# Performance work log

Hardware: AMD Instinct MI355X
Metric: run time of the kernel (lower is better)

Reference implementation:

```python
import jax, jax.numpy as jnp
import numpy as np

B, S, E, H = 32, 4096, 256, 8
P, M = 256, 16  # positions per batch row, tokens per position (pileup depth)


def setup_inputs() -> dict:
    key = jax.random.key(0)
    k1, k2, k3, k4, k5, k6 = jax.random.split(key, 6)
    embeddings = jax.random.normal(k1, (B, S, E), jnp.float32)
    # each position 0..P-1 appears exactly M times per batch row, shuffled
    base = jnp.repeat(jnp.arange(P, dtype=jnp.int32), M)  # (S,)
    positions = jax.vmap(lambda k: jax.random.permutation(k, base))(jax.random.split(k2, B))
    scale = 1.0 / np.sqrt(E)
    Wq = jax.random.normal(k3, (E, E), jnp.float32) * scale
    Wk = jax.random.normal(k4, (E, E), jnp.float32) * scale
    Wv = jax.random.normal(k5, (E, E), jnp.float32) * scale
    W0 = jax.random.normal(k6, (E, E), jnp.float32) * scale
    return {"embeddings": embeddings, "Wq": Wq, "Wk": Wk, "Wv": Wv, "W0": W0,
            "positions": positions, "num_positions": P, "group_size": M, "num_heads": H}


def _intra_group_rank(positions):
    # rank[b,i] = number of earlier tokens j<i in row b with the same position
    Bb, Ss = positions.shape
    idx = jnp.arange(Ss)
    order = jnp.argsort(positions, axis=1)  # stable sort preserves original order within a group
    sp = jnp.take_along_axis(positions, order, axis=1)
    new_group = jnp.concatenate([jnp.ones((Bb, 1), bool), sp[:, 1:] != sp[:, :-1]], axis=1)
    group_start = jax.lax.cummax(jnp.where(new_group, idx[None, :], 0), axis=1)
    rank_sorted = idx[None, :] - group_start
    rank = jnp.zeros_like(positions).at[jnp.arange(Bb)[:, None], order].set(rank_sorted.astype(positions.dtype))
    return rank


def reference(embeddings, Wq, Wk, Wv, W0, positions, num_positions, group_size, num_heads):
    Bb, Ss, Ee = embeddings.shape
    Pp, Mm, Hh = num_positions, group_size, num_heads
    dh = Ee // Hh
    G = Bb * Pp

    valid = positions >= 0
    rank = _intra_group_rank(positions)                       # (B,S) slot within group
    gid = jnp.arange(Bb, dtype=positions.dtype)[:, None] * Pp + jnp.clip(positions, 0)  # (B,S)
    gid_scat = jnp.where(valid, gid, G)                        # out-of-bounds -> dropped

    # gather: ragged regroup into (G, M, E), zero-padded like the torch version
    grouped = jnp.zeros((G, Mm, Ee), embeddings.dtype).at[gid_scat, rank].set(embeddings, mode='drop')

    # multi-head self-attention within each group (no mask, matching the original)
    q = (grouped @ Wq).reshape(G, Mm, Hh, dh)
    k = (grouped @ Wk).reshape(G, Mm, Hh, dh)
    v = (grouped @ Wv).reshape(G, Mm, Hh, dh)
    scores = jnp.einsum('gmhd,gnhd->ghmn', q, k) / np.sqrt(dh).astype(embeddings.dtype)
    attn = jax.nn.softmax(scores, axis=-1)
    ctx = jnp.einsum('ghmn,gnhd->gmhd', attn, v).reshape(G, Mm, Ee)
    att_out = ctx @ W0                                         # (G, M, E)

    # scatter back; invalid (-1) slots stay zero, as in the torch loop
    out = jnp.where(valid[:, :, None], att_out[gid, rank], 0.0)
    return out
```

## Files before the change

kernel.cpp:

```cpp
#include <hip/hip_runtime.h>
#include <stdint.h>

#define B_    32
#define S_    4096
#define E_    256
#define P_    256
#define M_    16
#define G_    (B_*P_)
#define NSLOT (G_*M_)
#define GPW   4
#define ROWS  64
#define NWG   (G_/GPW)

typedef float fv4 __attribute__((ext_vector_type(4)));
typedef int   iv4 __attribute__((ext_vector_type(4)));
typedef int   iv2 __attribute__((ext_vector_type(2)));
typedef __bf16 bv8 __attribute__((ext_vector_type(8)));
typedef short  sv4 __attribute__((ext_vector_type(4)));

__device__ __forceinline__ uint32_t bf16rne(float f) {
  uint32_t u = __builtin_bit_cast(uint32_t, f);
  u += 0x7fffu + ((u >> 16) & 1u);
  return u >> 16;
}
__device__ __forceinline__ uint32_t pk2(uint32_t lo, uint32_t hi) {
  return (lo & 0xffffu) | (hi << 16);
}
__device__ __forceinline__ void mfma32(fv4& d, iv4 a, iv4 b) {
  d = __builtin_amdgcn_mfma_f32_16x16x32_bf16(
        __builtin_bit_cast(bv8, a), __builtin_bit_cast(bv8, b), d, 0, 0, 0);
}
__device__ __forceinline__ void mfma16(fv4& d, iv2 a, iv2 b) {
  d = __builtin_amdgcn_mfma_f32_16x16x16bf16_1k(
        __builtin_bit_cast(sv4, a), __builtin_bit_cast(sv4, b), d, 0, 0, 0);
}
__device__ __forceinline__ void gload_lds16(const void* g, void* l) {
  __builtin_amdgcn_global_load_lds(
      (const __attribute__((address_space(1))) uint32_t*)g,
      (__attribute__((address_space(3))) uint32_t*)l, 16, 0, 0);
}

#define SWZ(off, row) ((off) ^ (((row) & 7) << 4))

__global__ void k_init(int* cnt, int* s2t) {
  int i = blockIdx.x * 256 + threadIdx.x;
  if (i < G_) cnt[i] = 0;
  if (i < NSLOT) s2t[i] = -1;
}

__global__ void k_trans(const float* __restrict__ Wq, const float* __restrict__ Wk,
                        const float* __restrict__ Wv, const float* __restrict__ W0,
                        uint16_t* __restrict__ WT) {
  int o = blockIdx.x * 256 + threadIdx.x;
  int wsel = blockIdx.y;
  const float* W = (wsel == 0) ? Wq : (wsel == 1) ? Wk : (wsel == 2) ? Wv : W0;
  int n = o >> 8, k = o & 255;
  WT[(size_t)wsel * 65536 + o] = (uint16_t)bf16rne(W[k * 256 + n]);
}

__global__ void k_rank(const int* __restrict__ pos, int* cnt, int* s2t) {
  int i = blockIdx.x * 256 + threadIdx.x;
  if (i >= B_ * S_) return;
  int p = pos[i];
  if (p < 0 || p >= P_) return;
  int b = i >> 12;
  int g = (b << 8) + p;
  int r = atomicAdd(&cnt[g], 1);
  if (r < M_) s2t[g * M_ + r] = i;
}

__global__ __launch_bounds__(512, 2) void k_main(
    const float* __restrict__ emb, const int* __restrict__ s2t,
    const uint16_t* __restrict__ WT, float* __restrict__ out) {
  extern __shared__ char smem[];
  char* buf0 = smem;
  char* Qb = smem + 32768;
  char* Kb = smem + 40960;
  char* Vb = smem + 49152;
  char* Cb = smem + 57344;

  const uint16_t* WqT = WT;
  const uint16_t* WkT = WT + 65536;
  const uint16_t* WvT = WT + 131072;
  const uint16_t* W0T = WT + 196608;

  const int tid = threadIdx.x;
  const int l = tid & 63;
  const int w = tid >> 6;
  const int lane15 = l & 15;
  const int lq = l >> 4;
  const int mq = w >> 1;
  const int nh = w & 1;
  const int slot0 = blockIdx.x * ROWS;

  #pragma unroll 2
  for (int rl = 0; rl < 8; ++rl) {
    int row = w * 8 + rl;
    int t = s2t[slot0 + row];
    uint32_t u0 = 0, u1 = 0;
    if (t >= 0) {
      const float4 v = *reinterpret_cast<const float4*>(emb + (size_t)t * E_ + (l << 2));
      u0 = pk2(bf16rne(v.x), bf16rne(v.y));
      u1 = pk2(bf16rne(v.z), bf16rne(v.w));
    }
    iv2 val; val[0] = (int)u0; val[1] = (int)u1;
    *reinterpret_cast<iv2*>(buf0 + row * 512 + SWZ(l * 8, row)) = val;
  }
  __syncthreads();

  iv4 xf[8];
  const int arow = mq * 16 + lane15;
  #pragma unroll
  for (int ks = 0; ks < 8; ++ks)
    xf[ks] = *reinterpret_cast<const iv4*>(buf0 + arow * 512 + SWZ(ks * 64 + lq * 16, arow));
  __syncthreads();

  fv4 outacc[8];
  #pragma unroll
  for (int i = 0; i < 8; ++i) outacc[i] = fv4{0.f, 0.f, 0.f, 0.f};

  for (int hc = 0; hc < 4; ++hc) {
    const int c0 = hc * 64;

    for (int wgt = 0; wgt < 3; ++wgt) {
      const uint16_t* Wt = (wgt == 0) ? WqT : (wgt == 1) ? WkT : WvT;
      char* dstb = (wgt == 0) ? Qb : (wgt == 1) ? Kb : Vb;
      #pragma unroll
      for (int it = 0; it < 4; ++it) {
        int q = it * 8 + w;
        int n = q * 2 + (l >> 5);
        int seg = l & 31;
        gload_lds16(reinterpret_cast<const char*>(Wt) + (size_t)(c0 + n) * 512 + SWZ(seg * 16, n),
                    buf0 + q * 1024);
      }
      __syncthreads();
      fv4 acc0 = fv4{0.f,0.f,0.f,0.f}, acc1 = fv4{0.f,0.f,0.f,0.f};
      const int n0 = nh * 32 + lane15, n1 = n0 + 16;
      #pragma unroll
      for (int ks = 0; ks < 8; ++ks) {
        iv4 b0 = *reinterpret_cast<const iv4*>(buf0 + n0 * 512 + SWZ(ks * 64 + lq * 16, n0));
        iv4 b1 = *reinterpret_cast<const iv4*>(buf0 + n1 * 512 + SWZ(ks * 64 + lq * 16, n1));
        mfma32(acc0, xf[ks], b0);
        mfma32(acc1, xf[ks], b1);
      }
      #pragma unroll
      for (int r = 0; r < 4; ++r) {
        int row = mq * 16 + lq * 4 + r;
        int col0 = nh * 32 + lane15;
        *reinterpret_cast<uint16_t*>(dstb + row * 128 + SWZ(col0 * 2, row)) =
            (uint16_t)bf16rne(acc0[r]);
        *reinterpret_cast<uint16_t*>(dstb + row * 128 + SWZ((col0 + 16) * 2, row)) =
            (uint16_t)bf16rne(acc1[r]);
      }
      __syncthreads();
    }

    #pragma unroll
    for (int it = 0; it < 4; ++it) {
      int q = it * 8 + w;
      int n = q * 8 + (l >> 3);
      int seg = l & 7;
      gload_lds16(reinterpret_cast<const char*>(W0T) + (size_t)n * 512 + (size_t)c0 * 2 + SWZ(seg * 16, n),
                  buf0 + q * 1024);
    }

    {
      int g = w >> 1, hh = w & 1;
      int rowb = g * 16;
      int frow = rowb + lane15;
      iv4 kf = *reinterpret_cast<const iv4*>(Kb + frow * 128 + SWZ(hh * 64 + lq * 16, frow));
      iv4 qf = *reinterpret_cast<const iv4*>(Qb + frow * 128 + SWZ(hh * 64 + lq * 16, frow));
      fv4 s = fv4{0.f, 0.f, 0.f, 0.f};
      mfma32(s, kf, qf);
      float mx = fmaxf(fmaxf(s[0], s[1]), fmaxf(s[2], s[3]));
      mx = fmaxf(mx, __shfl_xor(mx, 16));
      mx = fmaxf(mx, __shfl_xor(mx, 32));
      const float Cc = 0.25503373f;
      float e0 = exp2f((s[0] - mx) * Cc), e1 = exp2f((s[1] - mx) * Cc);
      float e2 = exp2f((s[2] - mx) * Cc), e3 = exp2f((s[3] - mx) * Cc);
      float sum = e0 + e1 + e2 + e3;
      sum += __shfl_xor(sum, 16);
      sum += __shfl_xor(sum, 32);
      float inv = 1.0f / sum;
      iv2 pa; pa[0] = (int)pk2(bf16rne(e0 * inv), bf16rne(e1 * inv));
              pa[1] = (int)pk2(bf16rne(e2 * inv), bf16rne(e3 * inv));
      #pragma unroll
      for (int dvt = 0; dvt < 2; ++dvt) {
        int col = hh * 32 + dvt * 16 + lane15;
        int r0 = rowb + lq * 4;
        uint32_t v0 = *reinterpret_cast<const uint16_t*>(Vb + (r0 + 0) * 128 + SWZ(col * 2, r0 + 0));
        uint32_t v1 = *reinterpret_cast<const uint16_t*>(Vb + (r0 + 1) * 128 + SWZ(col * 2, r0 + 1));
        uint32_t v2 = *reinterpret_cast<const uint16_t*>(Vb + (r0 + 2) * 128 + SWZ(col * 2, r0 + 2));
        uint32_t v3 = *reinterpret_cast<const uint16_t*>(Vb + (r0 + 3) * 128 + SWZ(col * 2, r0 + 3));
        iv2 bv; bv[0] = (int)pk2(v0, v1); bv[1] = (int)pk2(v2, v3);
        fv4 cacc = fv4{0.f, 0.f, 0.f, 0.f};
        mfma16(cacc, pa, bv);
        #pragma unroll
        for (int r = 0; r < 4; ++r) {
          int row = rowb + lq * 4 + r;
          *reinterpret_cast<uint16_t*>(Cb + row * 128 + SWZ(col * 2, row)) =
              (uint16_t)bf16rne(cacc[r]);
        }
      }
    }
    __syncthreads();

    #pragma unroll
    for (int ks = 0; ks < 2; ++ks) {
      int row = mq * 16 + lane15;
      iv4 af = *reinterpret_cast<const iv4*>(Cb + row * 128 + SWZ(ks * 64 + lq * 16, row));
      #pragma unroll
      for (int nt = 0; nt < 8; ++nt) {
        int n = nh * 128 + nt * 16 + lane15;
        iv4 bfg = *reinterpret_cast<const iv4*>(buf0 + n * 128 + SWZ(ks * 64 + lq * 16, n));
        mfma32(outacc[nt], af, bfg);
      }
    }
    __syncthreads();
  }

  #pragma unroll
  for (int r = 0; r < 4; ++r) {
    int t = s2t[slot0 + mq * 16 + lq * 4 + r];
    if (t < 0) continue;
    #pragma unroll
    for (int nt = 0; nt < 8; ++nt) {
      int col = nh * 128 + nt * 16 + lane15;
      out[(size_t)t * E_ + col] = outacc[nt][r];
    }
  }
}

extern "C" void kernel_launch(void* const* d_in, const int* in_sizes, int n_in,
                              void* d_out, int out_size, void* d_ws, size_t ws_size,
                              hipStream_t stream) {
  (void)in_sizes; (void)n_in; (void)out_size; (void)ws_size;
  const float* emb = (const float*)d_in[0];
  const float* Wq  = (const float*)d_in[1];
  const float* Wk  = (const float*)d_in[2];
  const float* Wv  = (const float*)d_in[3];
  const float* W0  = (const float*)d_in[4];
  const int*   pos = (const int*)d_in[5];
  float* out = (float*)d_out;

  int* cnt = (int*)d_ws;
  int* s2t = (int*)((char*)d_ws + 32768);
  uint16_t* WT = (uint16_t*)((char*)d_ws + 32768 + 524288);

  (void)hipFuncSetAttribute(reinterpret_cast<const void*>(k_main),
                            hipFuncAttributeMaxDynamicSharedMemorySize, 65536);

  k_init <<<512, 256, 0, stream>>>(cnt, s2t);
  k_trans<<<dim3(256, 4), 256, 0, stream>>>(Wq, Wk, Wv, W0, WT);
  k_rank <<<512, 256, 0, stream>>>(pos, cnt, s2t);
  k_main <<<NWG, 512, 65536, stream>>>(emb, s2t, WT, out);
}
```

Before: 220.3 us.

## Double-buffer weight staging and process 128 rows per workgroup

Each workgroup now handles 8 groups (128 rows) instead of 4, and the head loop is split into eight 32-column chunks. Weight tiles are double-buffered across two LDS buffers, and the next tile is prefetched with explicit vmcnt waits and raw barriers, so global-to-LDS loads overlap the MFMA work. The Q/K/V/C LDS layout is repacked to fit the narrower chunks. This cuts the number of workgroups and the weight reloads per row, and hides load latency. In exchange it needs more registers for a doubled output accumulator and relies on hand-written waitcnt ordering, which is fragile.

```diff
diff --git a/kernel.cpp b/kernel.cpp
--- a/kernel.cpp
+++ b/kernel.cpp
@@ -8,8 +8,8 @@
 #define M_    16
 #define G_    (B_*P_)
 #define NSLOT (G_*M_)
-#define GPW   4
-#define ROWS  64
+#define GPW   8
+#define ROWS  128
 #define NWG   (G_/GPW)
 
 typedef float fv4 __attribute__((ext_vector_type(4)));
@@ -41,6 +41,14 @@
 }
 
 #define SWZ(off, row) ((off) ^ (((row) & 7) << 4))
+#define LQKV(row, cb) ( ((row) >> 1) * 128 + \
+    (((((row) & 1) << 6) + (cb)) ^ ((((row) >> 1) & 7) << 4)) )
+
+#define BAR()   { asm volatile("" ::: "memory"); __builtin_amdgcn_s_barrier(); \
+                  asm volatile("" ::: "memory"); }
+#define VMWAIT2 asm volatile("s_waitcnt vmcnt(2)" ::: "memory")
+#define VMWAIT0 asm volatile("s_waitcnt vmcnt(0)" ::: "memory")
+#define LGKM0   asm volatile("s_waitcnt lgkmcnt(0)" ::: "memory")
 
 __global__ void k_init(int* cnt, int* s2t) {
   int i = blockIdx.x * 256 + threadIdx.x;
@@ -69,11 +77,36 @@
   if (r < M_) s2t[g * M_ + r] = i;
 }
 
+__device__ __forceinline__ void stage_qkv(const uint16_t* Wt, int c0, char* buf,
+                                          int w, int l) {
+  #pragma unroll
+  for (int it = 0; it < 2; ++it) {
+    int q = it * 8 + w;
+    int n = q * 2 + (l >> 5);
+    int seg = l & 31;
+    gload_lds16(reinterpret_cast<const char*>(Wt) + (size_t)(c0 + n) * 512 + SWZ(seg * 16, n),
+                buf + q * 1024);
+  }
+}
+__device__ __forceinline__ void stage_w0(const uint16_t* W0T, int c0, char* buf,
+                                         int w, int l) {
+  #pragma unroll
+  for (int it = 0; it < 2; ++it) {
+    int q = it * 8 + w;
+    int pair = q * 8 + (l >> 3);
+    int jp = ((l & 7) * 16) ^ ((pair & 7) << 4);
+    int n = 2 * pair + (jp >> 6);
+    gload_lds16(reinterpret_cast<const char*>(W0T) + (size_t)n * 512 + c0 * 2 + (jp & 63),
+                buf + q * 1024);
+  }
+}
+
 __global__ __launch_bounds__(512, 2) void k_main(
     const float* __restrict__ emb, const int* __restrict__ s2t,
     const uint16_t* __restrict__ WT, float* __restrict__ out) {
   extern __shared__ char smem[];
-  char* buf0 = smem;
+  char* bufA = smem;
+  char* bufB = smem + 16384;
   char* Qb = smem + 32768;
   char* Kb = smem + 40960;
   char* Vb = smem + 49152;
@@ -89,13 +122,13 @@
   const int w = tid >> 6;
   const int lane15 = l & 15;
   const int lq = l >> 4;
-  const int mq = w >> 1;
+  const int mq2 = w >> 1;
   const int nh = w & 1;
   const int slot0 = blockIdx.x * ROWS;
 
   #pragma unroll 2
-  for (int rl = 0; rl < 8; ++rl) {
-    int row = w * 8 + rl;
+  for (int rl = 0; rl < 16; ++rl) {
+    int row = w * 16 + rl;
     int t = s2t[slot0 + row];
     uint32_t u0 = 0, u1 = 0;
     if (t >= 0) {
@@ -104,72 +137,69 @@
       u1 = pk2(bf16rne(v.z), bf16rne(v.w));
     }
     iv2 val; val[0] = (int)u0; val[1] = (int)u1;
-    *reinterpret_cast<iv2*>(buf0 + row * 512 + SWZ(l * 8, row)) = val;
+    *reinterpret_cast<iv2*>(smem + row * 512 + SWZ(l * 8, row)) = val;
   }
   __syncthreads();
 
   iv4 xf[8];
-  const int arow = mq * 16 + lane15;
+  const int arow = w * 16 + lane15;
   #pragma unroll
   for (int ks = 0; ks < 8; ++ks)
-    xf[ks] = *reinterpret_cast<const iv4*>(buf0 + arow * 512 + SWZ(ks * 64 + lq * 16, arow));
+    xf[ks] = *reinterpret_cast<const iv4*>(smem + arow * 512 + SWZ(ks * 64 + lq * 16, arow));
   __syncthreads();
 
-  fv4 outacc[8];
-  #pragma unroll
-  for (int i = 0; i < 8; ++i) outacc[i] = fv4{0.f, 0.f, 0.f, 0.f};
-
-  for (int hc = 0; hc < 4; ++hc) {
-    const int c0 = hc * 64;
-
-    for (int wgt = 0; wgt < 3; ++wgt) {
-      const uint16_t* Wt = (wgt == 0) ? WqT : (wgt == 1) ? WkT : WvT;
-      char* dstb = (wgt == 0) ? Qb : (wgt == 1) ? Kb : Vb;
-      #pragma unroll
-      for (int it = 0; it < 4; ++it) {
-        int q = it * 8 + w;
-        int n = q * 2 + (l >> 5);
-        int seg = l & 31;
-        gload_lds16(reinterpret_cast<const char*>(Wt) + (size_t)(c0 + n) * 512 + SWZ(seg * 16, n),
-                    buf0 + q * 1024);
-      }
-      __syncthreads();
-      fv4 acc0 = fv4{0.f,0.f,0.f,0.f}, acc1 = fv4{0.f,0.f,0.f,0.f};
-      const int n0 = nh * 32 + lane15, n1 = n0 + 16;
-      #pragma unroll
-      for (int ks = 0; ks < 8; ++ks) {
-        iv4 b0 = *reinterpret_cast<const iv4*>(buf0 + n0 * 512 + SWZ(ks * 64 + lq * 16, n0));
-        iv4 b1 = *reinterpret_cast<const iv4*>(buf0 + n1 * 512 + SWZ(ks * 64 + lq * 16, n1));
-        mfma32(acc0, xf[ks], b0);
-        mfma32(acc1, xf[ks], b1);
-      }
-      #pragma unroll
-      for (int r = 0; r < 4; ++r) {
-        int row = mq * 16 + lq * 4 + r;
-        int col0 = nh * 32 + lane15;
-        *reinterpret_cast<uint16_t*>(dstb + row * 128 + SWZ(col0 * 2, row)) =
-            (uint16_t)bf16rne(acc0[r]);
-        *reinterpret_cast<uint16_t*>(dstb + row * 128 + SWZ((col0 + 16) * 2, row)) =
-            (uint16_t)bf16rne(acc1[r]);
-      }
-      __syncthreads();
-    }
-
+  fv4 outacc[2][8];
+  #pragma unroll
+  for (int a = 0; a < 2; ++a)
     #pragma unroll
-    for (int it = 0; it < 4; ++it) {
-      int q = it * 8 + w;
-      int n = q * 8 + (l >> 3);
-      int seg = l & 7;
-      gload_lds16(reinterpret_cast<const char*>(W0T) + (size_t)n * 512 + (size_t)c0 * 2 + SWZ(seg * 16, n),
-                  buf0 + q * 1024);
-    }
+    for (int b = 0; b < 8; ++b) outacc[a][b] = fv4{0.f, 0.f, 0.f, 0.f};
+
+  stage_qkv(WqT, 0, bufA, w, l);
+  stage_qkv(WkT, 0, bufB, w, l);
+
+  for (int hc = 0; hc < 8; ++hc) {
+    const int c0 = hc * 32;
+
+    #define COMPUTE_QKV(buf, dst)                                            \
+    {                                                                        \
+      fv4 a0 = fv4{0.f,0.f,0.f,0.f}, a1 = fv4{0.f,0.f,0.f,0.f};              \
+      const int n0 = lane15, n1 = lane15 + 16;                               \
+      _Pragma("unroll")                                                      \
+      for (int ks = 0; ks < 8; ++ks) {                                       \
+        iv4 b0 = *reinterpret_cast<const iv4*>((buf) + n0 * 512 + SWZ(ks * 64 + lq * 16, n0)); \
+        iv4 b1 = *reinterpret_cast<const iv4*>((buf) + n1 * 512 + SWZ(ks * 64 + lq * 16, n1)); \
+        mfma32(a0, xf[ks], b0);                                              \
+        mfma32(a1, xf[ks], b1);                                              \
+      }                                                                      \
+      _Pragma("unroll")                                                      \
+      for (int r = 0; r < 4; ++r) {                                          \
+        int row = w * 16 + lq * 4 + r;                                       \
+        *reinterpret_cast<uint16_t*>((dst) + LQKV(row, lane15 * 2)) =        \
+            (uint16_t)bf16rne(a0[r]);                                        \
+        *reinterpret_cast<uint16_t*>((dst) + LQKV(row, (lane15 + 16) * 2)) = \
+            (uint16_t)bf16rne(a1[r]);                                        \
+      }                                                                      \
+    }
+
+    VMWAIT2; BAR();
+    COMPUTE_QKV(bufA, Qb);
+    LGKM0; BAR();
+    stage_qkv(WvT, c0, bufA, w, l);
+
+    VMWAIT2; BAR();
+    COMPUTE_QKV(bufB, Kb);
+    LGKM0; BAR();
+    stage_w0(W0T, c0, bufB, w, l);
+
+    VMWAIT2; BAR();
+    COMPUTE_QKV(bufA, Vb);
+    LGKM0; BAR();
+    if (hc < 7) stage_qkv(WqT, c0 + 32, bufA, w, l);
 
     {
-      int g = w >> 1, hh = w & 1;
-      int rowb = g * 16;
-      int frow = rowb + lane15;
-      iv4 kf = *reinterpret_cast<const iv4*>(Kb + frow * 128 + SWZ(hh * 64 + lq * 16, frow));
-      iv4 qf = *reinterpret_cast<const iv4*>(Qb + frow * 128 + SWZ(hh * 64 + lq * 16, frow));
+      const int frow = w * 16 + lane15;
+      iv4 kf = *reinterpret_cast<const iv4*>(Kb + LQKV(frow, lq * 16));
+      iv4 qf = *reinterpret_cast<const iv4*>(Qb + LQKV(frow, lq * 16));
       fv4 s = fv4{0.f, 0.f, 0.f, 0.f};
       mfma32(s, kf, qf);
       float mx = fmaxf(fmaxf(s[0], s[1]), fmaxf(s[2], s[3]));
@@ -184,49 +214,57 @@
       float inv = 1.0f / sum;
       iv2 pa; pa[0] = (int)pk2(bf16rne(e0 * inv), bf16rne(e1 * inv));
               pa[1] = (int)pk2(bf16rne(e2 * inv), bf16rne(e3 * inv));
+      const int r0 = w * 16 + lq * 4;
       #pragma unroll
       for (int dvt = 0; dvt < 2; ++dvt) {
-        int col = hh * 32 + dvt * 16 + lane15;
-        int r0 = rowb + lq * 4;
-        uint32_t v0 = *reinterpret_cast<const uint16_t*>(Vb + (r0 + 0) * 128 + SWZ(col * 2, r0 + 0));
-        uint32_t v1 = *reinterpret_cast<const uint16_t*>(Vb + (r0 + 1) * 128 + SWZ(col * 2, r0 + 1));
-        uint32_t v2 = *reinterpret_cast<const uint16_t*>(Vb + (r0 + 2) * 128 + SWZ(col * 2, r0 + 2));
-        uint32_t v3 = *reinterpret_cast<const uint16_t*>(Vb + (r0 + 3) * 128 + SWZ(col * 2, r0 + 3));
+        int cb = (dvt * 16 + lane15) * 2;
+        uint32_t v0 = *reinterpret_cast<const uint16_t*>(Vb + LQKV(r0 + 0, cb));
+        uint32_t v1 = *reinterpret_cast<const uint16_t*>(Vb + LQKV(r0 + 1, cb));
+        uint32_t v2 = *reinterpret_cast<const uint16_t*>(Vb + LQKV(r0 + 2, cb));
+        uint32_t v3 = *reinterpret_cast<const uint16_t*>(Vb + LQKV(r0 + 3, cb));
         iv2 bv; bv[0] = (int)pk2(v0, v1); bv[1] = (int)pk2(v2, v3);
         fv4 cacc = fv4{0.f, 0.f, 0.f, 0.f};
         mfma16(cacc, pa, bv);
         #pragma unroll
-        for (int r = 0; r < 4; ++r) {
-          int row = rowb + lq * 4 + r;
-          *reinterpret_cast<uint16_t*>(Cb + row * 128 + SWZ(col * 2, row)) =
+        for (int r = 0; r < 4; ++r)
+          *reinterpret_cast<uint16_t*>(Cb + LQKV(r0 + r, cb)) =
               (uint16_t)bf16rne(cacc[r]);
-        }
       }
     }
-    __syncthreads();
-
+
+    if (hc < 7) { VMWAIT2; } else { VMWAIT0; }
+    LGKM0; BAR();
     #pragma unroll
-    for (int ks = 0; ks < 2; ++ks) {
-      int row = mq * 16 + lane15;
-      iv4 af = *reinterpret_cast<const iv4*>(Cb + row * 128 + SWZ(ks * 64 + lq * 16, row));
+    for (int mt = 0; mt < 2; ++mt) {
+      int ar = mq2 * 32 + mt * 16 + lane15;
+      iv4 af = *reinterpret_cast<const iv4*>(Cb + LQKV(ar, lq * 16));
       #pragma unroll
       for (int nt = 0; nt < 8; ++nt) {
         int n = nh * 128 + nt * 16 + lane15;
-        iv4 bfg = *reinterpret_cast<const iv4*>(buf0 + n * 128 + SWZ(ks * 64 + lq * 16, n));
-        mfma32(outacc[nt], af, bfg);
+        iv4 bfg = *reinterpret_cast<const iv4*>(
+            bufB + (n >> 1) * 128 + ((((n & 1) << 6) + lq * 16) ^ (((n >> 1) & 7) << 4)));
+        mfma32(outacc[mt][nt], af, bfg);
       }
     }
-    __syncthreads();
-  }
-
-  #pragma unroll
-  for (int r = 0; r < 4; ++r) {
-    int t = s2t[slot0 + mq * 16 + lq * 4 + r];
-    if (t < 0) continue;
+    BAR();
+    if (hc < 7) stage_qkv(WkT, c0 + 32, bufB, w, l);
+    #undef COMPUTE_QKV
+  }
+
+  #pragma unroll
+  for (int mt = 0; mt < 2; ++mt) {
+    int rb = mq2 * 32 + mt * 16 + lq * 4;
+    int t0 = s2t[slot0 + rb + 0];
+    int t1 = s2t[slot0 + rb + 1];
+    int t2 = s2t[slot0 + rb + 2];
+    int t3 = s2t[slot0 + rb + 3];
     #pragma unroll
     for (int nt = 0; nt < 8; ++nt) {
       int col = nh * 128 + nt * 16 + lane15;
-      out[(size_t)t * E_ + col] = outacc[nt][r];
+      if (t0 >= 0) out[(size_t)t0 * E_ + col] = outacc[mt][nt][0];
+      if (t1 >= 0) out[(size_t)t1 * E_ + col] = outacc[mt][nt][1];
+      if (t2 >= 0) out[(size_t)t2 * E_ + col] = outacc[mt][nt][2];
+      if (t3 >= 0) out[(size_t)t3 * E_ + col] = outacc[mt][nt][3];
     }
   }
 }
```

New measurement: 178.8 us. 1.23x faster.
